# Kernel optimization log

Measured on AMD Instinct MI355X. Metric: run time of the kernel, lower is better.

The kernel has to match this reference:

```python
import jax, jax.numpy as jnp
import numpy as np

S = 32      # stochastic size
D = 600     # deterministic size
H = 600     # hidden size
A = 6       # action size
E = 1024    # encoder embed size
T = 50      # steps
B = 1024    # batch
MIN_STD = 0.1


def setup_inputs() -> dict:
    key = jax.random.key(0)
    ks = jax.random.split(key, 20)
    p = lambda k, shp: (jax.random.normal(k, shp, dtype=jnp.float32) * 0.02)
    inp = {
        "steps": T,
        "encoded": jax.random.normal(ks[0], (T, B, E), dtype=jnp.float32),
        "actions": jax.random.normal(ks[1], (T, B, A), dtype=jnp.float32),
        "init_stoch": jnp.zeros((B, S), dtype=jnp.float32),
        "init_det": jnp.zeros((B, D), dtype=jnp.float32),
        "noise_prior": jax.random.normal(ks[2], (T, B, S), dtype=jnp.float32),
        "noise_post": jax.random.normal(ks[3], (T, B, S), dtype=jnp.float32),
        # transition model: rnn input MLP
        "W_in": p(ks[4], (H, A + S)), "b_in": jnp.zeros((H,), jnp.float32),
        # GRUCell (torch layout: gates r,z,n)
        "W_ih": p(ks[5], (3 * D, H)), "W_hh": p(ks[6], (3 * D, D)),
        "b_ih": jnp.zeros((3 * D,), jnp.float32), "b_hh": jnp.zeros((3 * D,), jnp.float32),
        # stochastic prior model
        "Wp1": p(ks[7], (H, D)), "bp1": jnp.zeros((H,), jnp.float32),
        "Wp2": p(ks[8], (2 * S, H)), "bp2": jnp.zeros((2 * S,), jnp.float32),
        # stochastic posterior model
        "Wq1": p(ks[9], (H, D + E)), "bq1": jnp.zeros((H,), jnp.float32),
        "Wq2": p(ks[10], (2 * S, H)), "bq2": jnp.zeros((2 * S,), jnp.float32),
    }
    return inp


def _rollout(encoded, actions, init_stoch, init_det, noise_prior, noise_post,
             W_in, b_in, W_ih, W_hh, b_ih, b_hh, Wp1, bp1, Wp2, bp2, Wq1, bq1, Wq2, bq2):
    elu = jax.nn.elu

    def gru_cell(x, h):
        gi = x @ W_ih.T + b_ih          # [B, 3D]
        gh = h @ W_hh.T + b_hh          # [B, 3D]
        ir, iz, inn = jnp.split(gi, 3, axis=-1)
        hr, hz, hn = jnp.split(gh, 3, axis=-1)
        r = jax.nn.sigmoid(ir + hr)
        z = jax.nn.sigmoid(iz + hz)
        n = jnp.tanh(inn + r * hn)
        return (1.0 - z) * n + z * h

    def step(carry, inp):
        stoch, det = carry
        enc_t, act_t, eps_p, eps_q = inp
        # transition model (prior)
        rnn_in = elu(jnp.concatenate([act_t, stoch], axis=-1) @ W_in.T + b_in)
        det_new = gru_cell(rnn_in, det)
        pm, ps_raw = jnp.split(elu(det_new @ Wp1.T + bp1) @ Wp2.T + bp2, 2, axis=-1)
        ps = jax.nn.softplus(ps_raw) + MIN_STD
        prior_stoch = pm + ps * eps_p
        # representation model (posterior)
        y = jnp.concatenate([det_new, enc_t], axis=-1)
        qm, qs_raw = jnp.split(elu(y @ Wq1.T + bq1) @ Wq2.T + bq2, 2, axis=-1)
        qs = jax.nn.softplus(qs_raw) + MIN_STD
        post_stoch = qm + qs * eps_q
        outs = (pm, ps, prior_stoch, det_new, qm, qs, post_stoch, det_new)
        return (post_stoch, det_new), outs

    _, outs = jax.lax.scan(step, (init_stoch, init_det),
                           (encoded, actions, noise_prior, noise_post))
    return outs  # each [T, B, *]


def reference(steps, encoded, actions, init_stoch, init_det, noise_prior, noise_post,
              W_in, b_in, W_ih, W_hh, b_ih, b_hh, Wp1, bp1, Wp2, bp2, Wq1, bq1, Wq2, bq2):
    # steps == T; scan rolls out the full horizon.
    return _rollout(encoded[:steps], actions[:steps], init_stoch, init_det,
                    noise_prior[:steps], noise_post[:steps],
                    W_in, b_in, W_ih, W_hh, b_ih, b_hh,
                    Wp1, bp1, Wp2, bp2, Wq1, bq1, Wq2, bq2)
```

## Files before the change

kernel.cpp:

```cpp
#include <hip/hip_runtime.h>

#define MFMA16 __builtin_amdgcn_mfma_f32_16x16x32_bf16

typedef __attribute__((ext_vector_type(8))) short short8;
typedef __attribute__((ext_vector_type(4))) float floatx4;

static constexpr int T_STEPS = 50;
static constexpr int BATCH   = 1024;
static constexpr int SDIM    = 32;
static constexpr int DDIM    = 600;
static constexpr int ADIM    = 6;
static constexpr int KP      = 608;
static constexpr int PITCH   = 616;
static constexpr int SAPITCH = 72;
static constexpr int NWAVES  = 10;
static constexpr int NTHREADS = 640;

static constexpr size_t SZ608    = (size_t)608 * 608;
static constexpr size_t OFF_WIHR = 0;
static constexpr size_t OFF_WIHZ = OFF_WIHR + SZ608;
static constexpr size_t OFF_WIHN = OFF_WIHZ + SZ608;
static constexpr size_t OFF_WHHR = OFF_WIHN + SZ608;
static constexpr size_t OFF_WHHZ = OFF_WHHR + SZ608;
static constexpr size_t OFF_WHHN = OFF_WHHZ + SZ608;
static constexpr size_t OFF_WP1  = OFF_WHHN + SZ608;
static constexpr size_t OFF_WQ1D = OFF_WP1  + SZ608;
static constexpr size_t OFF_WQ1E = OFF_WQ1D + SZ608;
static constexpr size_t OFF_WSA  = OFF_WQ1E + (size_t)608 * 1024;
static constexpr size_t OFF_WHEAD= OFF_WSA  + (size_t)608 * 64;
static constexpr size_t OFF_PREQ = OFF_WHEAD+ (size_t)128 * 608;
static constexpr size_t OFF_DETG = OFF_PREQ + (size_t)T_STEPS * BATCH * 600;
static constexpr size_t OFF_BAR  = OFF_DETG + (size_t)BATCH * KP;
static constexpr size_t OFF_PART = OFF_BAR + 256;

static constexpr size_t O_PM = 0;
static constexpr size_t O_PS = 1638400;
static constexpr size_t O_PR = 3276800;
static constexpr size_t O_D1 = 4915200;
static constexpr size_t O_QM = 35635200;
static constexpr size_t O_QS = 37273600;
static constexpr size_t O_PO = 38912000;
static constexpr size_t O_D2 = 40550400;

__device__ __forceinline__ unsigned short f2bf(float f) {
  unsigned u = __float_as_uint(f);
  u += 0x7FFFu + ((u >> 16) & 1u);
  return (unsigned short)(u >> 16);
}
__device__ __forceinline__ float bf2f(unsigned short u) {
  return __uint_as_float(((unsigned)u) << 16);
}
__device__ __forceinline__ float elu_f(float v) { return v > 0.f ? v : expm1f(v); }
__device__ __forceinline__ float sigmoid_f(float x) { return 1.f / (1.f + expf(-x)); }
__device__ __forceinline__ float tanh_f(float x) {
  x = fminf(fmaxf(x, -15.f), 15.f);
  float e = expf(2.f * x);
  return (e - 1.f) / (e + 1.f);
}

__global__ __launch_bounds__(256) void stage_weights(
    const float* __restrict__ Win, const float* __restrict__ Wih, const float* __restrict__ Whh,
    const float* __restrict__ Wp1, const float* __restrict__ Wq1,
    const float* __restrict__ Wp2, const float* __restrict__ Wq2,
    unsigned short* __restrict__ ws)
{
  const int region = blockIdx.y;
  if (region == 11) {
    if (blockIdx.x == 0 && threadIdx.x < 64)
      ((int*)(ws + OFF_BAR))[threadIdx.x] = 0;
    return;
  }
  int R = 608, C = 608;
  size_t dst = 0;
  switch (region) {
    case 0: dst = OFF_WIHR; break;
    case 1: dst = OFF_WIHZ; break;
    case 2: dst = OFF_WIHN; break;
    case 3: dst = OFF_WHHR; break;
    case 4: dst = OFF_WHHZ; break;
    case 5: dst = OFF_WHHN; break;
    case 6: dst = OFF_WP1;  break;
    case 7: dst = OFF_WQ1D; break;
    case 8: dst = OFF_WQ1E; C = 1024; break;
    case 9: dst = OFF_WSA;  C = 64;   break;
    case 10: dst = OFF_WHEAD; R = 128; break;
  }
  const int total = R * C;
  for (int e = blockIdx.x * 256 + threadIdx.x; e < total; e += gridDim.x * 256) {
    int n = e / C, k = e - n * C;
    float v = 0.f;
    switch (region) {
      case 0: if (n < 600 && k < 600) v = Wih[(size_t)n * 600 + k]; break;
      case 1: if (n < 600 && k < 600) v = Wih[(size_t)(600 + n) * 600 + k]; break;
      case 2: if (n < 600 && k < 600) v = Wih[(size_t)(1200 + n) * 600 + k]; break;
      case 3: if (n < 600 && k < 600) v = Whh[(size_t)n * 600 + k]; break;
      case 4: if (n < 600 && k < 600) v = Whh[(size_t)(600 + n) * 600 + k]; break;
      case 5: if (n < 600 && k < 600) v = Whh[(size_t)(1200 + n) * 600 + k]; break;
      case 6: if (n < 600 && k < 600) v = Wp1[(size_t)n * 600 + k]; break;
      case 7: if (n < 600 && k < 600) v = Wq1[(size_t)n * 1624 + k]; break;
      case 8: if (n < 600) v = Wq1[(size_t)n * 1624 + 600 + k]; break;
      case 9: if (n < 600) { if (k < 32) v = Win[(size_t)n * 38 + 6 + k];
                             else if (k < 38) v = Win[(size_t)n * 38 + (k - 32)]; } break;
      case 10: if (k < 600) v = (n < 64) ? Wp2[(size_t)n * 600 + k]
                                         : Wq2[(size_t)(n - 64) * 600 + k]; break;
    }
    ws[dst + (size_t)e] = f2bf(v);
  }
}

__global__ __launch_bounds__(256) void preq_gemm(
    const float* __restrict__ enc, const float* __restrict__ bq1,
    const unsigned short* __restrict__ ws, unsigned short* __restrict__ preq)
{
  __shared__ unsigned short A[16 * 1032];
  const size_t g0 = (size_t)blockIdx.x * 16;
  const int tid = threadIdx.x;

  const float4* e4 = (const float4*)(enc + g0 * 1024);
  for (int i = tid; i < 16 * 256; i += 256) {
    int row = i >> 8, c4 = i & 255;
    float4 v = e4[row * 256 + c4];
    int base = row * 1032 + c4 * 4;
    A[base + 0] = f2bf(v.x); A[base + 1] = f2bf(v.y);
    A[base + 2] = f2bf(v.z); A[base + 3] = f2bf(v.w);
  }
  __syncthreads();

  const int wave = tid >> 6, lane = tid & 63, q = lane >> 4, l15 = lane & 15;
  const unsigned short* Wq1e = ws + OFF_WQ1E;
  for (int tile = wave; tile < 38; tile += 4) {
    const int n0 = tile * 16;
    floatx4 acc = {0.f, 0.f, 0.f, 0.f};
    const unsigned short* wb = Wq1e + (size_t)(n0 + l15) * 1024 + q * 8;
    const int aoff = l15 * 1032 + q * 8;
    for (int ki = 0; ki < 32; ++ki) {
      short8 a = *(const short8*)(&A[aoff + ki * 32]);
      short8 b = *(const short8*)(wb + ki * 32);
      acc = MFMA16(a, b, acc, 0, 0, 0);
    }
    const int col = n0 + l15;
    if (col < 600) {
      float bb = bq1[col];
      for (int i = 0; i < 4; ++i) {
        int row = q * 4 + i;
        preq[(g0 + row) * 600 + col] = f2bf(acc[i] + bb);
      }
    }
  }
}

__global__ __launch_bounds__(NTHREADS)
__attribute__((amdgpu_waves_per_eu(2)))
void rssm_rollout(
    const float* __restrict__ actions, const float* __restrict__ init_stoch,
    const float* __restrict__ init_det,
    const float* __restrict__ eps_p, const float* __restrict__ eps_q,
    const float* __restrict__ b_in, const float* __restrict__ b_ih, const float* __restrict__ b_hh,
    const float* __restrict__ bp1, const float* __restrict__ bp2, const float* __restrict__ bq2,
    unsigned short* __restrict__ wsm, float* __restrict__ out)
{
  __shared__ unsigned short XB[16 * PITCH];
  __shared__ unsigned short DC[16 * PITCH];
  __shared__ unsigned short HQ[16 * PITCH];
  __shared__ unsigned short SA[16 * SAPITCH];

  const unsigned short* ws = wsm;
  const int tid  = threadIdx.x;
  const int wave = tid >> 6, lane = tid & 63, q = lane >> 4, l15 = lane & 15;
  const int wg    = blockIdx.x;
  const int slice = wg & 3;
  const int bg    = wg >> 2;
  const int brow0 = bg * 16;
  const int ntile = (slice < 3) ? 10 : 8;
  const int tile0 = slice * 10;
  const int cs    = slice * 160;

  unsigned short* DETG = wsm + OFF_DETG;
  int*   bar  = (int*)(wsm + OFF_BAR);
  float* PART = (float*)(wsm + OFF_PART);
  const unsigned short* preq = ws + OFF_PREQ;

  float* out_pm = out + O_PM; float* out_ps = out + O_PS; float* out_pr = out + O_PR;
  float* out_d1 = out + O_D1; float* out_qm = out + O_QM; float* out_qs = out + O_QS;
  float* out_po = out + O_PO; float* out_d2 = out + O_D2;

  int phase = 0;
  auto bgsync = [&]() {
    __syncthreads();
    ++phase;
    if (tid == 0) {
      __hip_atomic_fetch_add(&bar[bg], 1, __ATOMIC_RELAXED, __HIP_MEMORY_SCOPE_AGENT);
      while (__hip_atomic_load(&bar[bg], __ATOMIC_RELAXED, __HIP_MEMORY_SCOPE_AGENT) < 4 * phase)
        __builtin_amdgcn_s_sleep(2);
    }
    __syncthreads();
    asm volatile("" ::: "memory");
  };

  auto do_reduce = [&](int tcur) {
    const volatile float* part = (const volatile float*)(PART + (size_t)bg * (4 * 16 * 128));
    if (tid < 512) {
      const int r = tid >> 5, c = tid & 31;
      const volatile float* p0 = part + (0 * 16 + r) * 128;
      const volatile float* p1 = part + (1 * 16 + r) * 128;
      const volatile float* p2 = part + (2 * 16 + r) * 128;
      const volatile float* p3 = part + (3 * 16 + r) * 128;
      float a00 = p0[c], a01 = p0[32 + c], a02 = p0[64 + c], a03 = p0[96 + c];
      float a10 = p1[c], a11 = p1[32 + c], a12 = p1[64 + c], a13 = p1[96 + c];
      float a20 = p2[c], a21 = p2[32 + c], a22 = p2[64 + c], a23 = p2[96 + c];
      float a30 = p3[c], a31 = p3[32 + c], a32 = p3[64 + c], a33 = p3[96 + c];
      float pm  = bp2[c]      + a00 + a10 + a20 + a30;
      float psr = bp2[32 + c] + a01 + a11 + a21 + a31;
      float qm  = bq2[c]      + a02 + a12 + a22 + a32;
      float qsr = bq2[32 + c] + a03 + a13 + a23 + a33;
      const size_t oidx = ((size_t)(tcur - 1) * BATCH + brow0 + r) * SDIM + c;
      const float qs = (qsr > 30.f ? qsr : log1pf(expf(qsr))) + 0.1f;
      const float x  = qm + qs * eps_q[oidx];
      SA[r * SAPITCH + c] = f2bf(x);
      if (slice == 0) {
        const float ps = (psr > 30.f ? psr : log1pf(expf(psr))) + 0.1f;
        __builtin_nontemporal_store(pm, &out_pm[oidx]);
        __builtin_nontemporal_store(ps, &out_ps[oidx]);
        __builtin_nontemporal_store(pm + ps * eps_p[oidx], &out_pr[oidx]);
      } else if (slice == 1) {
        __builtin_nontemporal_store(qm, &out_qm[oidx]);
        __builtin_nontemporal_store(qs, &out_qs[oidx]);
        __builtin_nontemporal_store(x,  &out_po[oidx]);
      }
    }
  };

  for (int t = 0; t < T_STEPS; ++t) {
    if (t == 0) {
      for (int i = tid; i < 16 * PITCH; i += NTHREADS) { XB[i] = 0; DC[i] = 0; HQ[i] = 0; }
      for (int i = tid; i < 16 * SAPITCH; i += NTHREADS) SA[i] = 0;
      __syncthreads();
      for (int i = tid; i < 16 * SDIM; i += NTHREADS) {
        int r = i >> 5, c = i & 31;
        SA[r * SAPITCH + c] = f2bf(init_stoch[(size_t)(brow0 + r) * SDIM + c]);
      }
      for (int i = tid; i < 16 * DDIM; i += NTHREADS) {
        int r = i / DDIM, k = i - r * DDIM;
        DC[r * PITCH + k] = f2bf(init_det[(size_t)(brow0 + r) * DDIM + k]);
      }
      if (tid < 128) {
        int r = tid >> 3, c = 600 + (tid & 7);
        *(volatile unsigned short*)&DETG[(size_t)(brow0 + r) * KP + c] = 0;
      }
    } else {
      do_reduce(t);
    }
    if (tid < 96) {
      int r = tid / 6, j = tid - r * 6;
      SA[r * SAPITCH + 32 + j] = f2bf(actions[((size_t)t * BATCH + brow0 + r) * ADIM + j]);
    }
    __syncthreads();

    for (int tile = wave; tile < 38; tile += NWAVES) {
      const int n0 = tile * 16;
      floatx4 acc = {0.f, 0.f, 0.f, 0.f};
      const unsigned short* wb = ws + OFF_WSA + (size_t)(n0 + l15) * 64 + q * 8;
      const int aoff = l15 * SAPITCH + q * 8;
      short8 a0 = *(const short8*)(&SA[aoff]);
      short8 a1 = *(const short8*)(&SA[aoff + 32]);
      short8 b0 = *(const short8*)(wb);
      short8 b1 = *(const short8*)(wb + 32);
      acc = MFMA16(a0, b0, acc, 0, 0, 0);
      acc = MFMA16(a1, b1, acc, 0, 0, 0);
      const int col = n0 + l15;
      if (col < DDIM) {
        float bi = b_in[col];
        for (int i = 0; i < 4; ++i)
          XB[(q * 4 + i) * PITCH + col] = f2bf(elu_f(acc[i] + bi));
      }
    }
    __syncthreads();

    if (wave < ntile) {
      const int n0 = (tile0 + wave) * 16;
      floatx4 aIr = {0,0,0,0}, aIz = {0,0,0,0}, aIn = {0,0,0,0};
      floatx4 aHr = {0,0,0,0}, aHz = {0,0,0,0}, aHn = {0,0,0,0};
      const size_t wrow = (size_t)(n0 + l15) * KP + q * 8;
      const unsigned short* pIr = ws + OFF_WIHR + wrow;
      const unsigned short* pIz = ws + OFF_WIHZ + wrow;
      const unsigned short* pIn = ws + OFF_WIHN + wrow;
      const unsigned short* pHr = ws + OFF_WHHR + wrow;
      const unsigned short* pHz = ws + OFF_WHHZ + wrow;
      const unsigned short* pHn = ws + OFF_WHHN + wrow;
      const int aoff = l15 * PITCH + q * 8;
      short8 cIr, cIz, cIn, cHr, cHz, cHn;
      short8 nIr, nIz, nIn, nHr, nHz, nHn;
      cIr = *(const short8*)(pIr); cIz = *(const short8*)(pIz); cIn = *(const short8*)(pIn);
      cHr = *(const short8*)(pHr); cHz = *(const short8*)(pHz); cHn = *(const short8*)(pHn);
      #pragma unroll
      for (int ki = 0; ki < 19; ++ki) {
        if (ki < 18) {
          const int o = (ki + 1) * 32;
          nIr = *(const short8*)(pIr + o); nIz = *(const short8*)(pIz + o);
          nIn = *(const short8*)(pIn + o); nHr = *(const short8*)(pHr + o);
          nHz = *(const short8*)(pHz + o); nHn = *(const short8*)(pHn + o);
        }
        short8 ax = *(const short8*)(&XB[aoff + ki * 32]);
        short8 ad = *(const short8*)(&DC[aoff + ki * 32]);
        aIr = MFMA16(ax, cIr, aIr, 0, 0, 0);
        aIz = MFMA16(ax, cIz, aIz, 0, 0, 0);
        aIn = MFMA16(ax, cIn, aIn, 0, 0, 0);
        aHr = MFMA16(ad, cHr, aHr, 0, 0, 0);
        aHz = MFMA16(ad, cHz, aHz, 0, 0, 0);
        aHn = MFMA16(ad, cHn, aHn, 0, 0, 0);
        cIr = nIr; cIz = nIz; cIn = nIn; cHr = nHr; cHz = nHz; cHn = nHn;
      }
      const int d = n0 + l15;
      if (d < DDIM) {
        float bihr = b_ih[d],        bhhr = b_hh[d];
        float bihz = b_ih[600 + d],  bhhz = b_hh[600 + d];
        float bihn = b_ih[1200 + d], bhhn = b_hh[1200 + d];
        for (int i = 0; i < 4; ++i) {
          int row = q * 4 + i;
          float r = sigmoid_f(aIr[i] + aHr[i] + bihr + bhhr);
          float z = sigmoid_f(aIz[i] + aHz[i] + bihz + bhhz);
          float n = tanh_f(aIn[i] + bihn + r * (aHn[i] + bhhn));
          float dprev = bf2f(DC[row * PITCH + d]);
          float dn = (1.f - z) * n + z * dprev;
          *(volatile unsigned short*)&DETG[(size_t)(brow0 + row) * KP + d] = f2bf(dn);
          size_t oidx = ((size_t)t * BATCH + brow0 + row) * DDIM + d;
          __builtin_nontemporal_store(dn, &out_d1[oidx]);
          __builtin_nontemporal_store(dn, &out_d2[oidx]);
        }
      }
    }
    bgsync();

    {
      const volatile unsigned long long* src =
          (const volatile unsigned long long*)DETG;
      const int i0 = tid, i1 = tid + 640, i2 = tid + 1280, i3 = tid + 1920;
      const int r0 = i0 / 152, c0 = i0 - r0 * 152;
      const int r1 = i1 / 152, c1 = i1 - r1 * 152;
      const int r2 = i2 / 152, c2 = i2 - r2 * 152;
      const int r3 = i3 / 152, c3 = i3 - r3 * 152;
      unsigned long long v0, v1, v2, v3 = 0;
      v0 = src[(size_t)(brow0 + r0) * 152 + c0];
      v1 = src[(size_t)(brow0 + r1) * 152 + c1];
      v2 = src[(size_t)(brow0 + r2) * 152 + c2];
      if (i3 < 2432) v3 = src[(size_t)(brow0 + r3) * 152 + c3];
      *(unsigned long long*)(&DC[r0 * PITCH + c0 * 4]) = v0;
      *(unsigned long long*)(&DC[r1 * PITCH + c1 * 4]) = v1;
      *(unsigned long long*)(&DC[r2 * PITCH + c2 * 4]) = v2;
      if (i3 < 2432) *(unsigned long long*)(&DC[r3 * PITCH + c3 * 4]) = v3;
    }
    __syncthreads();

    if (wave < ntile) {
      const int n0 = (tile0 + wave) * 16;
      floatx4 accP = {0,0,0,0}, accQ = {0,0,0,0};
      const size_t wrow = (size_t)(n0 + l15) * KP + q * 8;
      const unsigned short* pP = ws + OFF_WP1  + wrow;
      const unsigned short* pQ = ws + OFF_WQ1D + wrow;
      const int aoff = l15 * PITCH + q * 8;
      short8 b0P, b0Q, b1P, b1Q, b2P, b2Q;
      b0P = *(const short8*)(pP);      b0Q = *(const short8*)(pQ);
      b1P = *(const short8*)(pP + 32); b1Q = *(const short8*)(pQ + 32);
      #pragma unroll
      for (int ki = 0; ki < 19; ++ki) {
        if (ki < 17) {
          const int o = (ki + 2) * 32;
          b2P = *(const short8*)(pP + o); b2Q = *(const short8*)(pQ + o);
        }
        short8 a = *(const short8*)(&DC[aoff + ki * 32]);
        accP = MFMA16(a, b0P, accP, 0, 0, 0);
        accQ = MFMA16(a, b0Q, accQ, 0, 0, 0);
        b0P = b1P; b0Q = b1Q; b1P = b2P; b1Q = b2Q;
      }
      const int col = n0 + l15;
      if (col < DDIM) {
        float bb = bp1[col];
        for (int i = 0; i < 4; ++i) {
          int row = q * 4 + i;
          XB[row * PITCH + col] = f2bf(elu_f(accP[i] + bb));
          float pre = bf2f(__builtin_nontemporal_load(
              &preq[((size_t)t * BATCH + brow0 + row) * 600 + col]));
          HQ[row * PITCH + col] = f2bf(elu_f(accQ[i] + pre));
        }
      }
    }
    __syncthreads();

    if (wave < 8) {
      const int h0 = wave * 16;
      const unsigned short* Asrc = (wave < 4) ? XB : HQ;
      floatx4 acc = {0,0,0,0};
      const unsigned short* pW = ws + OFF_WHEAD + (size_t)(h0 + l15) * KP + cs + q * 8;
      const int abase = l15 * PITCH + cs + q * 8;
      short8 w0, w1, w2, w3, w4 = {};
      short8 a0, a1, a2, a3, a4 = {};
      w0 = *(const short8*)(pW);       w1 = *(const short8*)(pW + 32);
      w2 = *(const short8*)(pW + 64);  w3 = *(const short8*)(pW + 96);
      a0 = *(const short8*)(&Asrc[abase]);      a1 = *(const short8*)(&Asrc[abase + 32]);
      a2 = *(const short8*)(&Asrc[abase + 64]); a3 = *(const short8*)(&Asrc[abase + 96]);
      if (slice < 3) {
        w4 = *(const short8*)(pW + 128);
        a4 = *(const short8*)(&Asrc[abase + 128]);
      }
      acc = MFMA16(a0, w0, acc, 0, 0, 0);
      acc = MFMA16(a1, w1, acc, 0, 0, 0);
      acc = MFMA16(a2, w2, acc, 0, 0, 0);
      acc = MFMA16(a3, w3, acc, 0, 0, 0);
      if (slice < 3) acc = MFMA16(a4, w4, acc, 0, 0, 0);
      volatile float* pdst = (volatile float*)(PART + (size_t)(bg * 4 + slice) * (16 * 128));
      for (int i = 0; i < 4; ++i)
        pdst[(q * 4 + i) * 128 + h0 + l15] = acc[i];
    }
    bgsync();
  }

  do_reduce(T_STEPS);
}

extern "C" void kernel_launch(void* const* d_in, const int* in_sizes, int n_in,
                              void* d_out, int out_size, void* d_ws, size_t ws_size,
                              hipStream_t stream) {
  const float* enc    = (const float*)d_in[1];
  const float* act    = (const float*)d_in[2];
  const float* init_s = (const float*)d_in[3];
  const float* init_d = (const float*)d_in[4];
  const float* np_    = (const float*)d_in[5];
  const float* nq_    = (const float*)d_in[6];
  const float* Win    = (const float*)d_in[7];
  const float* b_in   = (const float*)d_in[8];
  const float* Wih    = (const float*)d_in[9];
  const float* Whh    = (const float*)d_in[10];
  const float* bih    = (const float*)d_in[11];
  const float* bhh    = (const float*)d_in[12];
  const float* Wp1    = (const float*)d_in[13];
  const float* bp1    = (const float*)d_in[14];
  const float* Wp2    = (const float*)d_in[15];
  const float* bp2    = (const float*)d_in[16];
  const float* Wq1    = (const float*)d_in[17];
  const float* bq1    = (const float*)d_in[18];
  const float* Wq2    = (const float*)d_in[19];
  const float* bq2    = (const float*)d_in[20];
  unsigned short* ws  = (unsigned short*)d_ws;
  float* out = (float*)d_out;

  stage_weights<<<dim3(256, 12), 256, 0, stream>>>(Win, Wih, Whh, Wp1, Wq1, Wp2, Wq2, ws);
  preq_gemm<<<3200, 256, 0, stream>>>(enc, bq1, ws, ws + OFF_PREQ);
  rssm_rollout<<<256, NTHREADS, 0, stream>>>(act, init_s, init_d, np_, nq_,
                                             b_in, bih, bhh, bp1, bp2, bq2, ws, out);
}
```

Baseline: 3.618 ms.

## Split each batch group across eight workgroups with deeper weight prefetch

Result: slower. 6.074 ms (+67.9%).

```diff
diff --git a/kernel.cpp b/kernel.cpp
--- a/kernel.cpp
+++ b/kernel.cpp
@@ -1,6 +1,7 @@
 #include <hip/hip_runtime.h>
 
 #define MFMA16 __builtin_amdgcn_mfma_f32_16x16x32_bf16
+#define SGB    __builtin_amdgcn_sched_group_barrier
 
 typedef __attribute__((ext_vector_type(8))) short short8;
 typedef __attribute__((ext_vector_type(4))) float floatx4;
@@ -13,8 +14,8 @@
 static constexpr int KP      = 608;
 static constexpr int PITCH   = 616;
 static constexpr int SAPITCH = 72;
-static constexpr int NWAVES  = 10;
-static constexpr int NTHREADS = 640;
+static constexpr int NTHREADS = 512;
+static constexpr int NSLICE  = 8;
 
 static constexpr size_t SZ608    = (size_t)608 * 608;
 static constexpr size_t OFF_WIHR = 0;
@@ -150,7 +151,7 @@
 }
 
 __global__ __launch_bounds__(NTHREADS)
-__attribute__((amdgpu_waves_per_eu(2)))
+__attribute__((amdgpu_waves_per_eu(4)))
 void rssm_rollout(
     const float* __restrict__ actions, const float* __restrict__ init_stoch,
     const float* __restrict__ init_det,
@@ -168,12 +169,13 @@
   const int tid  = threadIdx.x;
   const int wave = tid >> 6, lane = tid & 63, q = lane >> 4, l15 = lane & 15;
   const int wg    = blockIdx.x;
-  const int slice = wg & 3;
-  const int bg    = wg >> 2;
+  const int slice = wg & 7;
+  const int bg    = wg >> 3;
   const int brow0 = bg * 16;
-  const int ntile = (slice < 3) ? 10 : 8;
-  const int tile0 = slice * 10;
-  const int cs    = slice * 160;
+  const int ntile = (slice < 6) ? 5 : 4;
+  const int tile0 = (slice < 6) ? slice * 5 : 30 + (slice - 6) * 4;
+  const int cs    = tile0 * 16;
+  const int Wd    = ntile * 16;
 
   unsigned short* DETG = wsm + OFF_DETG;
   int*   bar  = (int*)(wsm + OFF_BAR);
@@ -190,7 +192,7 @@
     ++phase;
     if (tid == 0) {
       __hip_atomic_fetch_add(&bar[bg], 1, __ATOMIC_RELAXED, __HIP_MEMORY_SCOPE_AGENT);
-      while (__hip_atomic_load(&bar[bg], __ATOMIC_RELAXED, __HIP_MEMORY_SCOPE_AGENT) < 4 * phase)
+      while (__hip_atomic_load(&bar[bg], __ATOMIC_RELAXED, __HIP_MEMORY_SCOPE_AGENT) < NSLICE * phase)
         __builtin_amdgcn_s_sleep(2);
     }
     __syncthreads();
@@ -198,30 +200,39 @@
   };
 
   auto do_reduce = [&](int tcur) {
-    const volatile float* part = (const volatile float*)(PART + (size_t)bg * (4 * 16 * 128));
-    if (tid < 512) {
+    const volatile float* part = (const volatile float*)(PART + (size_t)bg * (8 * 16 * 128));
+    {
       const int r = tid >> 5, c = tid & 31;
-      const volatile float* p0 = part + (0 * 16 + r) * 128;
-      const volatile float* p1 = part + (1 * 16 + r) * 128;
-      const volatile float* p2 = part + (2 * 16 + r) * 128;
-      const volatile float* p3 = part + (3 * 16 + r) * 128;
-      float a00 = p0[c], a01 = p0[32 + c], a02 = p0[64 + c], a03 = p0[96 + c];
-      float a10 = p1[c], a11 = p1[32 + c], a12 = p1[64 + c], a13 = p1[96 + c];
-      float a20 = p2[c], a21 = p2[32 + c], a22 = p2[64 + c], a23 = p2[96 + c];
-      float a30 = p3[c], a31 = p3[32 + c], a32 = p3[64 + c], a33 = p3[96 + c];
-      float pm  = bp2[c]      + a00 + a10 + a20 + a30;
-      float psr = bp2[32 + c] + a01 + a11 + a21 + a31;
-      float qm  = bq2[c]      + a02 + a12 + a22 + a32;
-      float qsr = bq2[32 + c] + a03 + a13 + a23 + a33;
+      const volatile float* P0 = part + (0 * 16 + r) * 128;
+      const volatile float* P1 = part + (1 * 16 + r) * 128;
+      const volatile float* P2 = part + (2 * 16 + r) * 128;
+      const volatile float* P3 = part + (3 * 16 + r) * 128;
+      const volatile float* P4 = part + (4 * 16 + r) * 128;
+      const volatile float* P5 = part + (5 * 16 + r) * 128;
+      const volatile float* P6 = part + (6 * 16 + r) * 128;
+      const volatile float* P7 = part + (7 * 16 + r) * 128;
+      float m0 = P0[c], s0 = P0[32+c], u0 = P0[64+c], v0 = P0[96+c];
+      float m1 = P1[c], s1 = P1[32+c], u1 = P1[64+c], v1 = P1[96+c];
+      float m2 = P2[c], s2 = P2[32+c], u2 = P2[64+c], v2 = P2[96+c];
+      float m3 = P3[c], s3 = P3[32+c], u3 = P3[64+c], v3 = P3[96+c];
+      float m4 = P4[c], s4 = P4[32+c], u4 = P4[64+c], v4 = P4[96+c];
+      float m5 = P5[c], s5 = P5[32+c], u5 = P5[64+c], v5 = P5[96+c];
+      float m6 = P6[c], s6 = P6[32+c], u6 = P6[64+c], v6 = P6[96+c];
+      float m7 = P7[c], s7 = P7[32+c], u7 = P7[64+c], v7 = P7[96+c];
+      float pm  = bp2[c]      + (((m0+m1)+(m2+m3)) + ((m4+m5)+(m6+m7)));
+      float psr = bp2[32 + c] + (((s0+s1)+(s2+s3)) + ((s4+s5)+(s6+s7)));
+      float qm  = bq2[c]      + (((u0+u1)+(u2+u3)) + ((u4+u5)+(u6+u7)));
+      float qsr = bq2[32 + c] + (((v0+v1)+(v2+v3)) + ((v4+v5)+(v6+v7)));
       const size_t oidx = ((size_t)(tcur - 1) * BATCH + brow0 + r) * SDIM + c;
       const float qs = (qsr > 30.f ? qsr : log1pf(expf(qsr))) + 0.1f;
-      const float x  = qm + qs * eps_q[oidx];
+      const float x  = qm + qs * __builtin_nontemporal_load(&eps_q[oidx]);
       SA[r * SAPITCH + c] = f2bf(x);
       if (slice == 0) {
         const float ps = (psr > 30.f ? psr : log1pf(expf(psr))) + 0.1f;
         __builtin_nontemporal_store(pm, &out_pm[oidx]);
         __builtin_nontemporal_store(ps, &out_ps[oidx]);
-        __builtin_nontemporal_store(pm + ps * eps_p[oidx], &out_pr[oidx]);
+        __builtin_nontemporal_store(pm + ps * __builtin_nontemporal_load(&eps_p[oidx]),
+                                    &out_pr[oidx]);
       } else if (slice == 1) {
         __builtin_nontemporal_store(qm, &out_qm[oidx]);
         __builtin_nontemporal_store(qs, &out_qs[oidx]);
@@ -256,7 +267,7 @@
     }
     __syncthreads();
 
-    for (int tile = wave; tile < 38; tile += NWAVES) {
+    for (int tile = wave; tile < 38; tile += 8) {
       const int n0 = tile * 16;
       floatx4 acc = {0.f, 0.f, 0.f, 0.f};
       const unsigned short* wb = ws + OFF_WSA + (size_t)(n0 + l15) * 64 + q * 8;
@@ -288,28 +299,33 @@
       const unsigned short* pHz = ws + OFF_WHHZ + wrow;
       const unsigned short* pHn = ws + OFF_WHHN + wrow;
       const int aoff = l15 * PITCH + q * 8;
-      short8 cIr, cIz, cIn, cHr, cHz, cHn;
-      short8 nIr, nIz, nIn, nHr, nHz, nHn;
-      cIr = *(const short8*)(pIr); cIz = *(const short8*)(pIz); cIn = *(const short8*)(pIn);
-      cHr = *(const short8*)(pHr); cHz = *(const short8*)(pHz); cHn = *(const short8*)(pHn);
+      short8 aIrc, aIzc, aInc, aHrc, aHzc, aHnc;
+      short8 bIrc, bIzc, bInc, bHrc, bHzc, bHnc;
+      short8 cIrc, cIzc, cInc, cHrc, cHzc, cHnc;
+#define LD6(S, o) \
+      S##Irc = *(const short8*)(pIr + (o)); S##Izc = *(const short8*)(pIz + (o)); \
+      S##Inc = *(const short8*)(pIn + (o)); S##Hrc = *(const short8*)(pHr + (o)); \
+      S##Hzc = *(const short8*)(pHz + (o)); S##Hnc = *(const short8*)(pHn + (o));
+      LD6(a, 0)
+      LD6(b, 32)
       #pragma unroll
       for (int ki = 0; ki < 19; ++ki) {
-        if (ki < 18) {
-          const int o = (ki + 1) * 32;
-          nIr = *(const short8*)(pIr + o); nIz = *(const short8*)(pIz + o);
-          nIn = *(const short8*)(pIn + o); nHr = *(const short8*)(pHr + o);
-          nHz = *(const short8*)(pHz + o); nHn = *(const short8*)(pHn + o);
-        }
+        if (ki < 17) { LD6(c, (ki + 2) * 32) }
         short8 ax = *(const short8*)(&XB[aoff + ki * 32]);
         short8 ad = *(const short8*)(&DC[aoff + ki * 32]);
-        aIr = MFMA16(ax, cIr, aIr, 0, 0, 0);
-        aIz = MFMA16(ax, cIz, aIz, 0, 0, 0);
-        aIn = MFMA16(ax, cIn, aIn, 0, 0, 0);
-        aHr = MFMA16(ad, cHr, aHr, 0, 0, 0);
-        aHz = MFMA16(ad, cHz, aHz, 0, 0, 0);
-        aHn = MFMA16(ad, cHn, aHn, 0, 0, 0);
-        cIr = nIr; cIz = nIz; cIn = nIn; cHr = nHr; cHz = nHz; cHn = nHn;
-      }
+        aIr = MFMA16(ax, aIrc, aIr, 0, 0, 0);
+        aIz = MFMA16(ax, aIzc, aIz, 0, 0, 0);
+        aIn = MFMA16(ax, aInc, aIn, 0, 0, 0);
+        aHr = MFMA16(ad, aHrc, aHr, 0, 0, 0);
+        aHz = MFMA16(ad, aHzc, aHz, 0, 0, 0);
+        aHn = MFMA16(ad, aHnc, aHn, 0, 0, 0);
+        SGB(0x20, 6, 0);
+        SGB(0x100, 2, 0);
+        SGB(0x8, 6, 0);
+        aIrc = bIrc; aIzc = bIzc; aInc = bInc; aHrc = bHrc; aHzc = bHzc; aHnc = bHnc;
+        bIrc = cIrc; bIzc = cIzc; bInc = cInc; bHrc = cHrc; bHzc = cHzc; bHnc = cHnc;
+      }
+#undef LD6
       const int d = n0 + l15;
       if (d < DDIM) {
         float bihr = b_ih[d],        bhhr = b_hh[d];
@@ -334,20 +350,23 @@
     {
       const volatile unsigned long long* src =
           (const volatile unsigned long long*)DETG;
-      const int i0 = tid, i1 = tid + 640, i2 = tid + 1280, i3 = tid + 1920;
+      const int i0 = tid, i1 = tid + 512, i2 = tid + 1024, i3 = tid + 1536, i4 = tid + 2048;
       const int r0 = i0 / 152, c0 = i0 - r0 * 152;
       const int r1 = i1 / 152, c1 = i1 - r1 * 152;
       const int r2 = i2 / 152, c2 = i2 - r2 * 152;
       const int r3 = i3 / 152, c3 = i3 - r3 * 152;
-      unsigned long long v0, v1, v2, v3 = 0;
+      const int r4 = i4 / 152, c4 = i4 - r4 * 152;
+      unsigned long long v0, v1, v2, v3, v4 = 0;
       v0 = src[(size_t)(brow0 + r0) * 152 + c0];
       v1 = src[(size_t)(brow0 + r1) * 152 + c1];
       v2 = src[(size_t)(brow0 + r2) * 152 + c2];
-      if (i3 < 2432) v3 = src[(size_t)(brow0 + r3) * 152 + c3];
+      v3 = src[(size_t)(brow0 + r3) * 152 + c3];
+      if (i4 < 2432) v4 = src[(size_t)(brow0 + r4) * 152 + c4];
       *(unsigned long long*)(&DC[r0 * PITCH + c0 * 4]) = v0;
       *(unsigned long long*)(&DC[r1 * PITCH + c1 * 4]) = v1;
       *(unsigned long long*)(&DC[r2 * PITCH + c2 * 4]) = v2;
-      if (i3 < 2432) *(unsigned long long*)(&DC[r3 * PITCH + c3 * 4]) = v3;
+      *(unsigned long long*)(&DC[r3 * PITCH + c3 * 4]) = v3;
+      if (i4 < 2432) *(unsigned long long*)(&DC[r4 * PITCH + c4 * 4]) = v4;
     }
     __syncthreads();
 
@@ -370,6 +389,9 @@
         short8 a = *(const short8*)(&DC[aoff + ki * 32]);
         accP = MFMA16(a, b0P, accP, 0, 0, 0);
         accQ = MFMA16(a, b0Q, accQ, 0, 0, 0);
+        SGB(0x20, 2, 0);
+        SGB(0x100, 1, 0);
+        SGB(0x8, 2, 0);
         b0P = b1P; b0Q = b1Q; b1P = b2P; b1Q = b2Q;
       }
       const int col = n0 + l15;
@@ -386,28 +408,28 @@
     }
     __syncthreads();
 
-    if (wave < 8) {
+    {
       const int h0 = wave * 16;
       const unsigned short* Asrc = (wave < 4) ? XB : HQ;
+      const int k0 = cs >> 5;
+      const unsigned short* pW = ws + OFF_WHEAD + (size_t)(h0 + l15) * KP + k0 * 32 + q * 8;
+      const int abase = l15 * PITCH + k0 * 32 + q * 8;
+      const int colq = k0 * 32 + q * 8;
+      short8 zz = {0, 0, 0, 0, 0, 0, 0, 0};
+      short8 a0 = *(const short8*)(&Asrc[abase]);
+      short8 a1 = *(const short8*)(&Asrc[abase + 32]);
+      short8 a2 = *(const short8*)(&Asrc[abase + 64]);
+      short8 w0 = *(const short8*)(pW);
+      short8 w1 = *(const short8*)(pW + 32);
+      short8 w2 = *(const short8*)(pW + 64);
+      if (colq      < cs || colq      >= cs + Wd) a0 = zz;
+      if (colq + 32 < cs || colq + 32 >= cs + Wd) a1 = zz;
+      if (colq + 64 < cs || colq + 64 >= cs + Wd) a2 = zz;
       floatx4 acc = {0,0,0,0};
-      const unsigned short* pW = ws + OFF_WHEAD + (size_t)(h0 + l15) * KP + cs + q * 8;
-      const int abase = l15 * PITCH + cs + q * 8;
-      short8 w0, w1, w2, w3, w4 = {};
-      short8 a0, a1, a2, a3, a4 = {};
-      w0 = *(const short8*)(pW);       w1 = *(const short8*)(pW + 32);
-      w2 = *(const short8*)(pW + 64);  w3 = *(const short8*)(pW + 96);
-      a0 = *(const short8*)(&Asrc[abase]);      a1 = *(const short8*)(&Asrc[abase + 32]);
-      a2 = *(const short8*)(&Asrc[abase + 64]); a3 = *(const short8*)(&Asrc[abase + 96]);
-      if (slice < 3) {
-        w4 = *(const short8*)(pW + 128);
-        a4 = *(const short8*)(&Asrc[abase + 128]);
-      }
       acc = MFMA16(a0, w0, acc, 0, 0, 0);
       acc = MFMA16(a1, w1, acc, 0, 0, 0);
       acc = MFMA16(a2, w2, acc, 0, 0, 0);
-      acc = MFMA16(a3, w3, acc, 0, 0, 0);
-      if (slice < 3) acc = MFMA16(a4, w4, acc, 0, 0, 0);
-      volatile float* pdst = (volatile float*)(PART + (size_t)(bg * 4 + slice) * (16 * 128));
+      volatile float* pdst = (volatile float*)(PART + (size_t)(bg * 8 + slice) * (16 * 128));
       for (int i = 0; i < 4; ++i)
         pdst[(q * 4 + i) * 128 + h0 + l15] = acc[i];
     }
@@ -445,6 +467,6 @@
 
   stage_weights<<<dim3(256, 12), 256, 0, stream>>>(Win, Wih, Whh, Wp1, Wq1, Wp2, Wq2, ws);
   preq_gemm<<<3200, 256, 0, stream>>>(enc, bq1, ws, ws + OFF_PREQ);
-  rssm_rollout<<<256, NTHREADS, 0, stream>>>(act, init_s, init_d, np_, nq_,
+  rssm_rollout<<<512, NTHREADS, 0, stream>>>(act, init_s, init_d, np_, nq_,
                                              b_in, bih, bhh, bp1, bp2, bq2, ws, out);
 }
```
